# Performance work log

Measured on AMD Instinct MI355X. Metric: run time of the kernel, lower is better.

The kernel has to match this reference:

```python
import jax, jax.numpy as jnp
import numpy as np

EPS = 1e-8  # torch.cosine_similarity default eps


def setup_inputs() -> dict:
    key = jax.random.key(0)
    k1, k2 = jax.random.split(key)
    B, S, C, W = 8, 75, 64, 19
    support_x = jax.random.normal(k1, (B, S, C, W, W), dtype=jnp.float32)
    query_x = jax.random.normal(k2, (B, S, C, W, W), dtype=jnp.float32)
    return {"support_x": support_x, "query_x": query_x}


def reference(support_x, query_x):
    # support_x, query_x: [B, S, C, W, W]
    # For each support spatial location (i,j), cosine-similarity of its C-vector
    # against every query spatial location (p,q), then max over (p,q).
    B, S, C, W, _ = support_x.shape
    s_norm = jnp.linalg.norm(support_x, axis=2)  # [B,S,W,W]
    q_norm = jnp.linalg.norm(query_x, axis=2)    # [B,S,W,W]
    # Pairwise dot products over channels: [B,S,Wi,Wj,Wp,Wq]
    num = jnp.einsum('bscij,bscpq->bsijpq', support_x, query_x)
    denom = jnp.maximum(s_norm[:, :, :, :, None, None] * q_norm[:, :, None, None, :, :], EPS)
    sim = num / denom
    out = jnp.max(sim, axis=(-2, -1))  # max over query spatial grid -> [B,S,W,W]
    # loop order was i (rows) then j (cols), concatenated on last dim == row-major reshape
    return out.reshape(B, S, W * W)
```

## Files before the change

kernel.cpp:

```cpp
#include <hip/hip_runtime.h>
#include <hip/hip_bf16.h>
#include <stdint.h>

#define WW    361
#define CCH   64
#define NTHR  256
#define WWC   (WW*CCH)
#define NOUT  (600*WW)

typedef __attribute__((ext_vector_type(8))) short short8;
typedef __attribute__((ext_vector_type(4))) float f32x4;


__device__ __forceinline__ unsigned int encf(float f) {
  unsigned int b = __float_as_uint(f);
  return (b & 0x80000000u) ? ~b : (b | 0x80000000u);
}

__device__ __forceinline__ float stage_row32(const float* __restrict__ gp,
                                             unsigned short* __restrict__ dst,
                                             int sw) {
  float ss = 0.f;
  #pragma unroll
  for (int h = 0; h < 2; ++h) {
    float v[32];
    #pragma unroll
    for (int j = 0; j < 32; ++j) v[j] = gp[(h * 32 + j) * WW];
    #pragma unroll
    for (int c = 0; c < 4; ++c) {
      unsigned int u[4];
      #pragma unroll
      for (int jj = 0; jj < 4; ++jj) {
        float x = v[c * 8 + 2 * jj], y = v[c * 8 + 2 * jj + 1];
        ss += x * x + y * y;
        __hip_bfloat162 b2 = __float22bfloat162_rn(make_float2(x, y));
        u[jj] = *(unsigned int*)&b2;
      }
      *(uint4*)&dst[((h * 4 + c) ^ sw) * 8] = make_uint4(u[0], u[1], u[2], u[3]);
    }
  }
  return rsqrtf(ss);
}

__device__ __forceinline__ void zero_row(unsigned short* __restrict__ dst) {
  #pragma unroll
  for (int c = 0; c < 8; ++c)
    *(uint4*)&dst[c * 8] = make_uint4(0u, 0u, 0u, 0u);
}

__device__ __forceinline__ void packA(const float* w, short8& af0, short8& af1,
                                      float& ssout) {
  unsigned int u[8];
  float ss = 0.f;
  #pragma unroll
  for (int jj = 0; jj < 8; ++jj) {
    float x = w[2 * jj], y = w[2 * jj + 1];
    ss += x * x + y * y;
    __hip_bfloat162 b2 = __float22bfloat162_rn(make_float2(x, y));
    u[jj] = *(unsigned int*)&b2;
  }
  uint4 t0 = make_uint4(u[0], u[1], u[2], u[3]);
  uint4 t1 = make_uint4(u[4], u[5], u[6], u[7]);
  af0 = *(short8*)&t0;
  af1 = *(short8*)&t1;
  ssout = ss;
}

__device__ __forceinline__ void epilogueAtomic(f32x4 mx, float invA, int tileBase,
                                               int quad, int l15,
                                               unsigned int* __restrict__ outb) {
  #pragma unroll
  for (int d = 1; d < 16; d <<= 1) {
    #pragma unroll
    for (int r = 0; r < 4; ++r) mx[r] = fmaxf(mx[r], __shfl_xor(mx[r], d));
  }
  const float iv0 = __shfl(invA, 4 * quad + 0);
  const float iv1 = __shfl(invA, 4 * quad + 1);
  const float iv2 = __shfl(invA, 4 * quad + 2);
  const float iv3 = __shfl(invA, 4 * quad + 3);
  if (l15 == 0) {
    const int mb = tileBase + 4 * quad;
    if (mb + 0 < WW) atomicMax(&outb[mb + 0], encf(mx[0] * iv0));
    if (mb + 1 < WW) atomicMax(&outb[mb + 1], encf(mx[1] * iv1));
    if (mb + 2 < WW) atomicMax(&outb[mb + 2], encf(mx[2] * iv2));
    if (mb + 3 < WW) atomicMax(&outb[mb + 3], encf(mx[3] * iv3));
  }
}

__global__ __launch_bounds__(NTHR, 4) void cossim_max_kernel(
    const float* __restrict__ support, const float* __restrict__ query,
    unsigned int* __restrict__ outenc)
{
  __shared__ __align__(16) unsigned short Q_sh[192 * CCH];
  __shared__ float inv_q[192];

  const int tid  = threadIdx.x;
  const int lane = tid & 63;
  const int wv   = tid >> 6;
  const int l15  = lane & 15;
  const int quad = lane >> 4;

  const int b  = ((int)blockIdx.x & 7) * 300 + ((int)blockIdx.x >> 3);
  const int bs = b >> 2;
  const int qh = b & 1;
  const int ih = (b >> 1) & 1;
  const int qBase = qh * 192;
  const int mBase = ih * 192;

  const float* sg = support + (size_t)bs * WWC;
  const float* qg = query   + (size_t)bs * WWC;

  const int nreal = qh ? (WW - 192) : 192;
  if (tid < 192) {
    if (tid < nreal) {
      inv_q[tid] = stage_row32(qg + qBase + tid, &Q_sh[tid * CCH], tid & 7);
    } else if (tid < 176) {
      zero_row(&Q_sh[tid * CCH]);
      inv_q[tid] = 0.f;
    }
  }

  short8 af[3][2]; float invA[3];
  {
    const int iG0 = mBase + 16 * (3 * wv + 0) + l15;
    const int iG1 = mBase + 16 * (3 * wv + 1) + l15;
    const int iG2 = mBase + 16 * (3 * wv + 2) + l15;
    const bool v0 = iG0 < WW, v1 = iG1 < WW, v2 = iG2 < WW;
    float ss0, ss1, ss2;
    {
      float w[32];
      const float* s0 = sg + iG0;
      const float* s1 = sg + iG1;
      if (v0) {
        #pragma unroll
        for (int j = 0; j < 8; ++j) w[j]     = s0[(8 * quad + j) * WW];
        #pragma unroll
        for (int j = 0; j < 8; ++j) w[8 + j] = s0[(32 + 8 * quad + j) * WW];
      } else {
        #pragma unroll
        for (int j = 0; j < 16; ++j) w[j] = 0.f;
      }
      if (v1) {
        #pragma unroll
        for (int j = 0; j < 8; ++j) w[16 + j] = s1[(8 * quad + j) * WW];
        #pragma unroll
        for (int j = 0; j < 8; ++j) w[24 + j] = s1[(32 + 8 * quad + j) * WW];
      } else {
        #pragma unroll
        for (int j = 0; j < 16; ++j) w[16 + j] = 0.f;
      }
      packA(&w[0],  af[0][0], af[0][1], ss0);
      packA(&w[16], af[1][0], af[1][1], ss1);
    }
    {
      float w[16];
      const float* s2 = sg + iG2;
      if (v2) {
        #pragma unroll
        for (int j = 0; j < 8; ++j) w[j]     = s2[(8 * quad + j) * WW];
        #pragma unroll
        for (int j = 0; j < 8; ++j) w[8 + j] = s2[(32 + 8 * quad + j) * WW];
      } else {
        #pragma unroll
        for (int j = 0; j < 16; ++j) w[j] = 0.f;
      }
      packA(&w[0], af[2][0], af[2][1], ss2);
    }
    ss0 += __shfl_xor(ss0, 16); ss0 += __shfl_xor(ss0, 32);
    ss1 += __shfl_xor(ss1, 16); ss1 += __shfl_xor(ss1, 32);
    ss2 += __shfl_xor(ss2, 16); ss2 += __shfl_xor(ss2, 32);
    invA[0] = v0 ? rsqrtf(ss0) : 0.f;
    invA[1] = v1 ? rsqrtf(ss1) : 0.f;
    invA[2] = v2 ? rsqrtf(ss2) : 0.f;
  }

  __syncthreads();

  const int boff0 = l15 * CCH + ((quad       ^ (l15 & 7)) * 8);
  const int boff1 = l15 * CCH + (((4 + quad) ^ (l15 & 7)) * 8);
  const int NTB = qh ? 11 : 12;
  const float lastbias = (qh && l15 >= 9) ? -1e30f : 0.f;

  f32x4 mx0 = {-3e38f, -3e38f, -3e38f, -3e38f};
  f32x4 mx1 = mx0, mx2 = mx0;

  for (int t = 0; t < NTB; ++t) {
    const int nb = t * 16 * CCH;
    short8 b0 = *(const short8*)&Q_sh[nb + boff0];
    short8 b1 = *(const short8*)&Q_sh[nb + boff1];
    const float qs = inv_q[t * 16 + l15];
    const float bb = (t == NTB - 1) ? lastbias : 0.f;
    f32x4 a0 = {0.f, 0.f, 0.f, 0.f}, a1 = a0, a2 = a0;
    __builtin_amdgcn_s_setprio(1);
    a0 = __builtin_amdgcn_mfma_f32_16x16x32_bf16(af[0][0], b0, a0, 0, 0, 0);
    a0 = __builtin_amdgcn_mfma_f32_16x16x32_bf16(af[0][1], b1, a0, 0, 0, 0);
    a1 = __builtin_amdgcn_mfma_f32_16x16x32_bf16(af[1][0], b0, a1, 0, 0, 0);
    a1 = __builtin_amdgcn_mfma_f32_16x16x32_bf16(af[1][1], b1, a1, 0, 0, 0);
    a2 = __builtin_amdgcn_mfma_f32_16x16x32_bf16(af[2][0], b0, a2, 0, 0, 0);
    a2 = __builtin_amdgcn_mfma_f32_16x16x32_bf16(af[2][1], b1, a2, 0, 0, 0);
    __builtin_amdgcn_s_setprio(0);
    #pragma unroll
    for (int r = 0; r < 4; ++r) {
      mx0[r] = fmaxf(mx0[r], a0[r] * qs + bb);
      mx1[r] = fmaxf(mx1[r], a1[r] * qs + bb);
      mx2[r] = fmaxf(mx2[r], a2[r] * qs + bb);
    }
  }

  unsigned int* outb = outenc + (size_t)bs * WW;
  epilogueAtomic(mx0, invA[0], mBase + 16 * (3 * wv + 0), quad, l15, outb);
  epilogueAtomic(mx1, invA[1], mBase + 16 * (3 * wv + 1), quad, l15, outb);
  epilogueAtomic(mx2, invA[2], mBase + 16 * (3 * wv + 2), quad, l15, outb);
}

__global__ void cossim_decode(unsigned int* __restrict__ p) {
  const int i = blockIdx.x * blockDim.x + threadIdx.x;
  if (i < NOUT) {
    const unsigned int u = p[i];
    p[i] = (u & 0x80000000u) ? (u & 0x7fffffffu) : ~u;
  }
}

extern "C" void kernel_launch(void* const* d_in, const int* in_sizes, int n_in,
                              void* d_out, int out_size, void* d_ws, size_t ws_size,
                              hipStream_t stream) {
  const float* support = (const float*)d_in[0];
  const float* query   = (const float*)d_in[1];
  unsigned int* outenc = (unsigned int*)d_out;
  hipMemsetAsync(d_out, 0, (size_t)out_size, stream);
  dim3 grid(2400), block(NTHR);
  hipLaunchKernelGGL(cossim_max_kernel, grid, block, 0, stream,
                     support, query, outenc);
  dim3 dgrid((NOUT + 255) / 256), dblock(256);
  hipLaunchKernelGGL(cossim_decode, dgrid, dblock, 0, stream, outenc);
}
```

Baseline: 151.7 us.

## Process each (batch,sample) pair in one block and drop atomics/memset/decode

Each block now handles a whole (b,s) pair with 512 threads. It stages all 361 query rows (padded to 368) in LDS and covers all support rows across 8 waves, instead of splitting the pair into four quarter-blocks. This halves global reads of support and query. It also removes the cross-block atomicMax, the output memset and the decode kernel, so results are written as plain float stores in a single launch. The trade-off is fewer blocks (600 versus 2400) and larger LDS use per block, which may reduce occupancy and cause load imbalance across CUs.

```diff
diff --git a/kernel.cpp b/kernel.cpp
--- a/kernel.cpp
+++ b/kernel.cpp
@@ -4,18 +4,14 @@
 
 #define WW    361
 #define CCH   64
-#define NTHR  256
+#define NQR   368
+#define NT    23
+#define NTHR  512
 #define WWC   (WW*CCH)
-#define NOUT  (600*WW)
 
 typedef __attribute__((ext_vector_type(8))) short short8;
 typedef __attribute__((ext_vector_type(4))) float f32x4;
 
-
-__device__ __forceinline__ unsigned int encf(float f) {
-  unsigned int b = __float_as_uint(f);
-  return (b & 0x80000000u) ? ~b : (b | 0x80000000u);
-}
 
 __device__ __forceinline__ float stage_row32(const float* __restrict__ gp,
                                              unsigned short* __restrict__ dst,
@@ -66,9 +62,9 @@
   ssout = ss;
 }
 
-__device__ __forceinline__ void epilogueAtomic(f32x4 mx, float invA, int tileBase,
-                                               int quad, int l15,
-                                               unsigned int* __restrict__ outb) {
+__device__ __forceinline__ void epilogueStore(f32x4 mx, float invA, int tileBase,
+                                              int quad, int l15,
+                                              float* __restrict__ outb) {
   #pragma unroll
   for (int d = 1; d < 16; d <<= 1) {
     #pragma unroll
@@ -80,19 +76,19 @@
   const float iv3 = __shfl(invA, 4 * quad + 3);
   if (l15 == 0) {
     const int mb = tileBase + 4 * quad;
-    if (mb + 0 < WW) atomicMax(&outb[mb + 0], encf(mx[0] * iv0));
-    if (mb + 1 < WW) atomicMax(&outb[mb + 1], encf(mx[1] * iv1));
-    if (mb + 2 < WW) atomicMax(&outb[mb + 2], encf(mx[2] * iv2));
-    if (mb + 3 < WW) atomicMax(&outb[mb + 3], encf(mx[3] * iv3));
-  }
-}
-
-__global__ __launch_bounds__(NTHR, 4) void cossim_max_kernel(
+    if (mb + 0 < WW) outb[mb + 0] = mx[0] * iv0;
+    if (mb + 1 < WW) outb[mb + 1] = mx[1] * iv1;
+    if (mb + 2 < WW) outb[mb + 2] = mx[2] * iv2;
+    if (mb + 3 < WW) outb[mb + 3] = mx[3] * iv3;
+  }
+}
+
+__global__ __launch_bounds__(NTHR, 6) void cossim_max_kernel(
     const float* __restrict__ support, const float* __restrict__ query,
-    unsigned int* __restrict__ outenc)
+    float* __restrict__ out)
 {
-  __shared__ __align__(16) unsigned short Q_sh[192 * CCH];
-  __shared__ float inv_q[192];
+  __shared__ __align__(16) unsigned short Q_sh[NQR * CCH];
+  __shared__ float inv_q[NQR];
 
   const int tid  = threadIdx.x;
   const int lane = tid & 63;
@@ -100,21 +96,14 @@
   const int l15  = lane & 15;
   const int quad = lane >> 4;
 
-  const int b  = ((int)blockIdx.x & 7) * 300 + ((int)blockIdx.x >> 3);
-  const int bs = b >> 2;
-  const int qh = b & 1;
-  const int ih = (b >> 1) & 1;
-  const int qBase = qh * 192;
-  const int mBase = ih * 192;
-
+  const int bs = (int)blockIdx.x;
   const float* sg = support + (size_t)bs * WWC;
   const float* qg = query   + (size_t)bs * WWC;
 
-  const int nreal = qh ? (WW - 192) : 192;
-  if (tid < 192) {
-    if (tid < nreal) {
-      inv_q[tid] = stage_row32(qg + qBase + tid, &Q_sh[tid * CCH], tid & 7);
-    } else if (tid < 176) {
+  if (tid < NQR) {
+    if (tid < WW) {
+      inv_q[tid] = stage_row32(qg + tid, &Q_sh[tid * CCH], tid & 7);
+    } else {
       zero_row(&Q_sh[tid * CCH]);
       inv_q[tid] = 0.f;
     }
@@ -122,9 +111,9 @@
 
   short8 af[3][2]; float invA[3];
   {
-    const int iG0 = mBase + 16 * (3 * wv + 0) + l15;
-    const int iG1 = mBase + 16 * (3 * wv + 1) + l15;
-    const int iG2 = mBase + 16 * (3 * wv + 2) + l15;
+    const int iG0 = 16 * (3 * wv + 0) + l15;
+    const int iG1 = 16 * (3 * wv + 1) + l15;
+    const int iG2 = 16 * (3 * wv + 2) + l15;
     const bool v0 = iG0 < WW, v1 = iG1 < WW, v2 = iG2 < WW;
     float ss0, ss1, ss2;
     {
@@ -178,18 +167,17 @@
 
   const int boff0 = l15 * CCH + ((quad       ^ (l15 & 7)) * 8);
   const int boff1 = l15 * CCH + (((4 + quad) ^ (l15 & 7)) * 8);
-  const int NTB = qh ? 11 : 12;
-  const float lastbias = (qh && l15 >= 9) ? -1e30f : 0.f;
+  const float lastbias = (l15 < 9) ? 0.f : -1e30f;
 
   f32x4 mx0 = {-3e38f, -3e38f, -3e38f, -3e38f};
   f32x4 mx1 = mx0, mx2 = mx0;
 
-  for (int t = 0; t < NTB; ++t) {
+  for (int t = 0; t < NT; ++t) {
     const int nb = t * 16 * CCH;
     short8 b0 = *(const short8*)&Q_sh[nb + boff0];
     short8 b1 = *(const short8*)&Q_sh[nb + boff1];
     const float qs = inv_q[t * 16 + l15];
-    const float bb = (t == NTB - 1) ? lastbias : 0.f;
+    const float bb = (t == NT - 1) ? lastbias : 0.f;
     f32x4 a0 = {0.f, 0.f, 0.f, 0.f}, a1 = a0, a2 = a0;
     __builtin_amdgcn_s_setprio(1);
     a0 = __builtin_amdgcn_mfma_f32_16x16x32_bf16(af[0][0], b0, a0, 0, 0, 0);
@@ -207,17 +195,14 @@
     }
   }
 
-  unsigned int* outb = outenc + (size_t)bs * WW;
-  epilogueAtomic(mx0, invA[0], mBase + 16 * (3 * wv + 0), quad, l15, outb);
-  epilogueAtomic(mx1, invA[1], mBase + 16 * (3 * wv + 1), quad, l15, outb);
-  epilogueAtomic(mx2, invA[2], mBase + 16 * (3 * wv + 2), quad, l15, outb);
-}
-
-__global__ void cossim_decode(unsigned int* __restrict__ p) {
-  const int i = blockIdx.x * blockDim.x + threadIdx.x;
-  if (i < NOUT) {
-    const unsigned int u = p[i];
-    p[i] = (u & 0x80000000u) ? (u & 0x7fffffffu) : ~u;
+  float* outb = out + (size_t)bs * WW;
+  {
+    const int tb0 = 16 * (3 * wv + 0);
+    const int tb1 = 16 * (3 * wv + 1);
+    const int tb2 = 16 * (3 * wv + 2);
+    if (tb0 < WW) epilogueStore(mx0, invA[0], tb0, quad, l15, outb);
+    if (tb1 < WW) epilogueStore(mx1, invA[1], tb1, quad, l15, outb);
+    if (tb2 < WW) epilogueStore(mx2, invA[2], tb2, quad, l15, outb);
   }
 }
 
@@ -226,11 +211,8 @@
                               hipStream_t stream) {
   const float* support = (const float*)d_in[0];
   const float* query   = (const float*)d_in[1];
-  unsigned int* outenc = (unsigned int*)d_out;
-  hipMemsetAsync(d_out, 0, (size_t)out_size, stream);
-  dim3 grid(2400), block(NTHR);
+  float* out = (float*)d_out;
+  dim3 grid(600), block(NTHR);
   hipLaunchKernelGGL(cossim_max_kernel, grid, block, 0, stream,
-                     support, query, outenc);
-  dim3 dgrid((NOUT + 255) / 256), dblock(256);
-  hipLaunchKernelGGL(cossim_decode, dgrid, dblock, 0, stream, outenc);
-}
+                     support, query, out);
+}
```

After: 294.3 us. 1.94x slower.
